# Optimization experiments

Measured on AMD Instinct MI355X. Metric: run time of the kernel, lower is better.

The kernel has to match this reference:

```python
import jax, jax.numpy as jnp
import numpy as np

B, L, DIM = 2, 2048, 768
NH, HD = 12, 64  # num_heads, head_dim; NH*HD == dim_attn == 768


def setup_inputs() -> dict:
    key = jax.random.key(0)
    ks = jax.random.split(key, 7)
    x = jax.random.normal(ks[0], (B, L, DIM), dtype=jnp.float32)
    pos_bias = jax.random.normal(ks[1], (1, NH, L, L), dtype=jnp.float32)
    Wq = jax.random.normal(ks[2], (DIM, DIM), dtype=jnp.float32) * 0.02
    Wk = jax.random.normal(ks[3], (DIM, DIM), dtype=jnp.float32) * 0.02
    Wv = jax.random.normal(ks[4], (DIM, DIM), dtype=jnp.float32) * 0.02
    Wo = jax.random.normal(ks[5], (DIM, DIM), dtype=jnp.float32) * 0.02
    mask = jax.random.randint(ks[6], (B, L), 0, 2, dtype=jnp.int32)
    return {"x": x, "pos_bias": pos_bias, "Wq": Wq, "Wk": Wk, "Wv": Wv,
            "Wo": Wo, "mask": mask}


def reference(x, pos_bias, Wq, Wk, Wv, Wo, mask):
    b, l, _ = x.shape
    # q/k/v projections (torch Linear: x @ W.T), split into heads
    q = (x @ Wq.T).reshape(b, l, NH, HD)
    k = (x @ Wk.T).reshape(b, l, NH, HD)
    v = (x @ Wv.T).reshape(b, l, NH, HD)
    # additive bias [B, H, Lq, Lk]: pos_bias broadcast + key mask -> -inf
    neg_inf = jnp.finfo(x.dtype).min
    attn_bias = jnp.broadcast_to(pos_bias, (b, NH, l, l))
    attn_bias = jnp.where(mask[:, None, None, :] == 0, neg_inf, attn_bias)
    # T5-style attention: NO 1/sqrt(d) scaling
    scores = jnp.einsum('binc,bjnc->bnij', q, k) + attn_bias
    attn = jax.nn.softmax(scores.astype(jnp.float32), axis=-1).astype(x.dtype)
    out = jnp.einsum('bnij,bjnc->binc', attn, v).reshape(b, l, NH * HD)
    return out @ Wo.T
```

## Files before the change

### kernel.cpp

```cpp
#include <hip/hip_runtime.h>
#include <math.h>

#define Bq 2
#define Lq 2048
#define DIMq 768
#define NHq 12
#define HDq 64

typedef __attribute__((ext_vector_type(8))) short short8;
typedef __attribute__((ext_vector_type(4))) short short4v;
typedef __attribute__((ext_vector_type(4))) float float4v;

static __device__ __forceinline__ short f2bf(float f) {
    union { float f; unsigned u; } v; v.f = f;
    unsigned r = (v.u + 0x7FFF + ((v.u >> 16) & 1)) >> 16;
    return (short)r;
}

__global__ __launch_bounds__(256)
void to_bf16(const float* __restrict__ x,  const float* __restrict__ wq,
             const float* __restrict__ wk, const float* __restrict__ wv,
             const float* __restrict__ wo,
             short* __restrict__ xb, short* __restrict__ wqb,
             short* __restrict__ wkb, short* __restrict__ wvb,
             short* __restrict__ wob)
{
    int blk = blockIdx.x;
    const float* s; short* d; int off;
    if      (blk <  768) { s = x;  d = xb;  off = blk * 1024; }
    else if (blk <  912) { s = wq; d = wqb; off = (blk -  768) * 1024; }
    else if (blk < 1056) { s = wk; d = wkb; off = (blk -  912) * 1024; }
    else if (blk < 1200) { s = wv; d = wvb; off = (blk - 1056) * 1024; }
    else                 { s = wo; d = wob; off = (blk - 1200) * 1024; }
    const float4* s4 = (const float4*)s;
    short4v* d4 = (short4v*)d;
#pragma unroll
    for (int i = 0; i < 4; ++i) {
        int idx = off + threadIdx.x + i * 256;
        float4 v = s4[idx];
        short4v o;
        o[0] = f2bf(v.x); o[1] = f2bf(v.y); o[2] = f2bf(v.z); o[3] = f2bf(v.w);
        d4[idx] = o;
    }
}

__global__ __launch_bounds__(256, 2)
void gemm_bf16(const short* __restrict__ A,
               const short* __restrict__ W0, const short* __restrict__ W1,
               const short* __restrict__ W2,
               short* __restrict__ D0, short* __restrict__ D1,
               short* __restrict__ D2, float* __restrict__ DF, int mode)
{
    const int z = blockIdx.z;
    const short* W = (z == 0) ? W0 : ((z == 1) ? W1 : W2);
    short* DH = (z == 0) ? D0 : ((z == 1) ? D1 : D2);

    __shared__ __align__(16) short Xs[64][72];
    __shared__ __align__(16) short Ws[64][72];

    const int tid  = threadIdx.x;
    const int wave = tid >> 6;
    const int lane = tid & 63;
    const int col  = lane & 15;
    const int quad = lane >> 4;
    const int m0 = blockIdx.y * 64, n0 = blockIdx.x * 64;

    float4v acc[4];
#pragma unroll
    for (int nt = 0; nt < 4; ++nt) acc[nt] = (float4v){0.f, 0.f, 0.f, 0.f};

    for (int k0 = 0; k0 < DIMq; k0 += 64) {
        __syncthreads();
#pragma unroll
        for (int i = 0; i < 2; ++i) {
            int idx = tid + i * 256;
            int mm = idx >> 3, ch = idx & 7;
            *(short8*)&Xs[mm][ch * 8] =
                *(const short8*)&A[(size_t)(m0 + mm) * DIMq + k0 + ch * 8];
            *(short8*)&Ws[mm][ch * 8] =
                *(const short8*)&W[(size_t)(n0 + mm) * DIMq + k0 + ch * 8];
        }
        __syncthreads();
#pragma unroll
        for (int kk = 0; kk < 2; ++kk) {
            short8 a = *(const short8*)&Xs[wave * 16 + col][kk * 32 + quad * 8];
#pragma unroll
            for (int nt = 0; nt < 4; ++nt) {
                short8 bfr = *(const short8*)&Ws[nt * 16 + col][kk * 32 + quad * 8];
                acc[nt] = __builtin_amdgcn_mfma_f32_16x16x32_bf16(a, bfr, acc[nt], 0, 0, 0);
            }
        }
    }

#pragma unroll
    for (int reg = 0; reg < 4; ++reg) {
        int m = m0 + wave * 16 + quad * 4 + reg;
#pragma unroll
        for (int nt = 0; nt < 4; ++nt) {
            int n = n0 + 16 * nt + col;
            if (mode == 1) {
                int b = m >> 11, l = m & 2047, h = n >> 6, c = n & 63;
                DH[(((size_t)(b * NHq + h)) * Lq + l) * HDq + c] = f2bf(acc[nt][reg]);
            } else {
                DF[(size_t)m * DIMq + n] = acc[nt][reg];
            }
        }
    }
}

__global__ __launch_bounds__(256, 2)
void attn_fwd_mfma(const short* __restrict__ Qh, const short* __restrict__ Kh,
                   const short* __restrict__ Vh, const float* __restrict__ pos_bias,
                   const int* __restrict__ mask, short* __restrict__ AO)
{
    const int qt = blockIdx.x;
    const int h  = blockIdx.y;
    const int b  = blockIdx.z;
    const short* Q = Qh + ((size_t)(b * NHq + h)) * Lq * HDq;
    const short* K = Kh + ((size_t)(b * NHq + h)) * Lq * HDq;
    const short* V = Vh + ((size_t)(b * NHq + h)) * Lq * HDq;
    const int* mk = mask + (size_t)b * Lq;

    __shared__ __align__(16) short Ks[64][72];
    __shared__ __align__(16) short Vt[64][72];
    __shared__ __align__(16) short Ps[64][72];

    const int tid  = threadIdx.x;
    const int wave = tid >> 6;
    const int lane = tid & 63;
    const int col  = lane & 15;
    const int quad = lane >> 4;

    short8 qa[2];
    {
        const short* qrow = Q + (size_t)(qt * 64 + wave * 16 + col) * HDq;
        qa[0] = *(const short8*)&qrow[quad * 8];
        qa[1] = *(const short8*)&qrow[32 + quad * 8];
    }

    const float* brow = pos_bias + (size_t)h * Lq * Lq
                      + (size_t)(qt * 64 + wave * 16 + quad * 4) * Lq + col;

    float bcur[4][4], bnxt[4][4];
    auto prefetch = [&](int kt, float (&bb)[4][4]) {
#pragma unroll
        for (int nt = 0; nt < 4; ++nt) {
            int mval = mk[kt * 64 + col + 16 * nt];
            float fm = (mval == 0) ? -1e30f : 0.0f;
#pragma unroll
            for (int reg = 0; reg < 4; ++reg)
                bb[nt][reg] = brow[(size_t)reg * Lq + kt * 64 + 16 * nt] + fm;
        }
    };
    prefetch(0, bcur);

    float4v Oacc[4];
    float m_run[4], l_run[4];
#pragma unroll
    for (int nt = 0; nt < 4; ++nt) Oacc[nt] = (float4v){0.f, 0.f, 0.f, 0.f};
#pragma unroll
    for (int r = 0; r < 4; ++r) { m_run[r] = -1e30f; l_run[r] = 0.f; }

    for (int kt = 0; kt < Lq / 64; ++kt) {
        __syncthreads();
        const short* Kt = K + (size_t)kt * 64 * HDq;
        const short* Vg = V + (size_t)kt * 64 * HDq;
#pragma unroll
        for (int i = 0; i < 2; ++i) {
            int idx = tid + i * 256;
            int key = idx >> 3, ch = idx & 7;
            *(short8*)&Ks[key][ch * 8] = *(const short8*)&Kt[key * HDq + ch * 8];
        }
        {
            int key = tid & 63, hg = tid >> 6;
#pragma unroll
            for (int i = 0; i < 2; ++i) {
                int c = hg + i * 4;
                short8 vv = *(const short8*)&Vg[key * HDq + c * 8];
#pragma unroll
                for (int j = 0; j < 8; ++j)
                    Vt[c * 8 + j][key] = vv[j];
            }
        }
        if (kt + 1 < Lq / 64) prefetch(kt + 1, bnxt);
        __syncthreads();

        float4v S[4];
#pragma unroll
        for (int nt = 0; nt < 4; ++nt) S[nt] = (float4v){0.f, 0.f, 0.f, 0.f};
#pragma unroll
        for (int kk = 0; kk < 2; ++kk) {
#pragma unroll
            for (int nt = 0; nt < 4; ++nt) {
                short8 bfr = *(const short8*)&Ks[nt * 16 + col][kk * 32 + quad * 8];
                S[nt] = __builtin_amdgcn_mfma_f32_16x16x32_bf16(qa[kk], bfr, S[nt], 0, 0, 0);
            }
        }

        float sc[4][4];
#pragma unroll
        for (int nt = 0; nt < 4; ++nt)
#pragma unroll
            for (int reg = 0; reg < 4; ++reg)
                sc[nt][reg] = S[nt][reg] + bcur[nt][reg];
        float tm[4];
#pragma unroll
        for (int reg = 0; reg < 4; ++reg) {
            tm[reg] = fmaxf(fmaxf(sc[0][reg], sc[1][reg]),
                            fmaxf(sc[2][reg], sc[3][reg]));
#pragma unroll
            for (int off = 1; off < 16; off <<= 1)
                tm[reg] = fmaxf(tm[reg], __shfl_xor(tm[reg], off, 64));
        }
        float alpha[4], ps[4];
#pragma unroll
        for (int reg = 0; reg < 4; ++reg) {
            float mn = fmaxf(m_run[reg], tm[reg]);
            alpha[reg] = __expf(m_run[reg] - mn);
            m_run[reg] = mn;
            ps[reg] = 0.f;
        }
#pragma unroll
        for (int nt = 0; nt < 4; ++nt)
#pragma unroll
            for (int reg = 0; reg < 4; ++reg) {
                float p = __expf(sc[nt][reg] - m_run[reg]);
                sc[nt][reg] = p;
                ps[reg] += p;
            }
#pragma unroll
        for (int reg = 0; reg < 4; ++reg) {
#pragma unroll
            for (int off = 1; off < 16; off <<= 1)
                ps[reg] += __shfl_xor(ps[reg], off, 64);
            l_run[reg] = l_run[reg] * alpha[reg] + ps[reg];
        }
#pragma unroll
        for (int nt = 0; nt < 4; ++nt)
#pragma unroll
            for (int reg = 0; reg < 4; ++reg)
                Ps[wave * 16 + quad * 4 + reg][col + 16 * nt] = f2bf(sc[nt][reg]);
#pragma unroll
        for (int nt = 0; nt < 4; ++nt)
#pragma unroll
            for (int reg = 0; reg < 4; ++reg)
                Oacc[nt][reg] *= alpha[reg];
        __syncthreads();

#pragma unroll
        for (int kk = 0; kk < 2; ++kk) {
            short8 pa = *(const short8*)&Ps[wave * 16 + col][kk * 32 + quad * 8];
#pragma unroll
            for (int nt = 0; nt < 4; ++nt) {
                short8 vb = *(const short8*)&Vt[nt * 16 + col][kk * 32 + quad * 8];
                Oacc[nt] = __builtin_amdgcn_mfma_f32_16x16x32_bf16(pa, vb, Oacc[nt], 0, 0, 0);
            }
        }
#pragma unroll
        for (int nt = 0; nt < 4; ++nt)
#pragma unroll
            for (int reg = 0; reg < 4; ++reg)
                bcur[nt][reg] = bnxt[nt][reg];
    }

    short* aorow = AO + ((size_t)b * Lq + qt * 64 + wave * 16 + quad * 4) * DIMq
                 + h * HDq + col;
#pragma unroll
    for (int reg = 0; reg < 4; ++reg) {
        float inv = 1.0f / l_run[reg];
#pragma unroll
        for (int nt = 0; nt < 4; ++nt)
            aorow[(size_t)reg * DIMq + 16 * nt] = f2bf(Oacc[nt][reg] * inv);
    }
}

extern "C" void kernel_launch(void* const* d_in, const int* in_sizes, int n_in,
                              void* d_out, int out_size, void* d_ws, size_t ws_size,
                              hipStream_t stream) {
    const float* x        = (const float*)d_in[0];
    const float* pos_bias = (const float*)d_in[1];
    const float* Wq       = (const float*)d_in[2];
    const float* Wk       = (const float*)d_in[3];
    const float* Wv       = (const float*)d_in[4];
    const float* Wo       = (const float*)d_in[5];
    const int*   mask     = (const int*)d_in[6];
    float* out = (float*)d_out;

    const size_t nX = (size_t)Bq * Lq * DIMq;
    const size_t nW = (size_t)DIMq * DIMq;
    short* xb  = (short*)d_ws;
    short* wqb = xb  + nX;
    short* wkb = wqb + nW;
    short* wvb = wkb + nW;
    short* wob = wvb + nW;
    short* Qh  = wob + nW;
    short* Kh  = Qh  + nX;
    short* Vh  = Kh  + nX;
    short* AOb = Vh  + nX;

    dim3 blk(256);
    hipLaunchKernelGGL(to_bf16, dim3(1344), blk, 0, stream,
                       x, Wq, Wk, Wv, Wo, xb, wqb, wkb, wvb, wob);

    hipLaunchKernelGGL(gemm_bf16, dim3(DIMq / 64, (Bq * Lq) / 64, 3), blk, 0, stream,
                       xb, wqb, wkb, wvb, Qh, Kh, Vh, (float*)nullptr, 1);

    hipLaunchKernelGGL(attn_fwd_mfma, dim3(Lq / 64, NHq, Bq), blk, 0, stream,
                       Qh, Kh, Vh, pos_bias, mask, AOb);

    hipLaunchKernelGGL(gemm_bf16, dim3(DIMq / 64, (Bq * Lq) / 64, 1), blk, 0, stream,
                       AOb, wob, wob, wob, (short*)nullptr, (short*)nullptr,
                       (short*)nullptr, out, 0);
}
```

Baseline: 429.1 us.

## Use 128x128 GEMM tiles with direct global-to-LDS loads and double-buffer attention K/V

The GEMM moves from 64x64 to 128x128 output tiles, with each wave computing a 64x64 sub-tile, and fills LDS with global_load_lds instead of staging through registers. The aim is more operand reuse per MFMA and fewer load instructions. The attention kernel double-buffers K and V in LDS, loading the next tile into registers while the current tile is computed and writing it to LDS after the PV MFMAs, which cuts one barrier per iteration. In exchange the GEMM uses more registers, and with unpadded LDS rows its fragment reads may hit bank conflicts. The GEMM grid also shrinks, so fewer blocks are in flight.

```diff
diff --git a/kernel.cpp b/kernel.cpp
--- a/kernel.cpp
+++ b/kernel.cpp
@@ -11,10 +11,17 @@
 typedef __attribute__((ext_vector_type(4))) short short4v;
 typedef __attribute__((ext_vector_type(4))) float float4v;
 
+typedef __attribute__((address_space(3))) unsigned int as3_u32;
+typedef __attribute__((address_space(1))) unsigned int as1_u32;
+
 static __device__ __forceinline__ short f2bf(float f) {
     union { float f; unsigned u; } v; v.f = f;
     unsigned r = (v.u + 0x7FFF + ((v.u >> 16) & 1)) >> 16;
     return (short)r;
+}
+
+static __device__ __forceinline__ void gld_lds16(const short* g, short* l) {
+    __builtin_amdgcn_global_load_lds((const as1_u32*)g, (as3_u32*)l, 16, 0, 0);
 }
 
 __global__ __launch_bounds__(256)
@@ -55,54 +62,67 @@
     const short* W = (z == 0) ? W0 : ((z == 1) ? W1 : W2);
     short* DH = (z == 0) ? D0 : ((z == 1) ? D1 : D2);
 
-    __shared__ __align__(16) short Xs[64][72];
-    __shared__ __align__(16) short Ws[64][72];
+    __shared__ __align__(16) short As[128][64];
+    __shared__ __align__(16) short Ws[128][64];
 
     const int tid  = threadIdx.x;
     const int wave = tid >> 6;
     const int lane = tid & 63;
     const int col  = lane & 15;
     const int quad = lane >> 4;
-    const int m0 = blockIdx.y * 64, n0 = blockIdx.x * 64;
-
-    float4v acc[4];
-#pragma unroll
-    for (int nt = 0; nt < 4; ++nt) acc[nt] = (float4v){0.f, 0.f, 0.f, 0.f};
+    const int wr = wave >> 1, wc = wave & 1;
+    const int m0 = blockIdx.y * 128, n0 = blockIdx.x * 128;
+
+    float4v acc[4][4];
+#pragma unroll
+    for (int mt = 0; mt < 4; ++mt)
+#pragma unroll
+        for (int nt = 0; nt < 4; ++nt) acc[mt][nt] = (float4v){0.f, 0.f, 0.f, 0.f};
+
+    const short* Ab = A + (size_t)m0 * DIMq;
+    const short* Wb = W + (size_t)n0 * DIMq;
 
     for (int k0 = 0; k0 < DIMq; k0 += 64) {
         __syncthreads();
 #pragma unroll
-        for (int i = 0; i < 2; ++i) {
-            int idx = tid + i * 256;
-            int mm = idx >> 3, ch = idx & 7;
-            *(short8*)&Xs[mm][ch * 8] =
-                *(const short8*)&A[(size_t)(m0 + mm) * DIMq + k0 + ch * 8];
-            *(short8*)&Ws[mm][ch * 8] =
-                *(const short8*)&W[(size_t)(n0 + mm) * DIMq + k0 + ch * 8];
+        for (int i = 0; i < 4; ++i) {
+            int g = i * 256 + tid;
+            int row = g >> 3, ch = g & 7;
+            gld_lds16(Ab + (size_t)row * DIMq + k0 + ch * 8, (short*)As + g * 8);
+            gld_lds16(Wb + (size_t)row * DIMq + k0 + ch * 8, (short*)Ws + g * 8);
         }
         __syncthreads();
 #pragma unroll
         for (int kk = 0; kk < 2; ++kk) {
-            short8 a = *(const short8*)&Xs[wave * 16 + col][kk * 32 + quad * 8];
-#pragma unroll
-            for (int nt = 0; nt < 4; ++nt) {
-                short8 bfr = *(const short8*)&Ws[nt * 16 + col][kk * 32 + quad * 8];
-                acc[nt] = __builtin_amdgcn_mfma_f32_16x16x32_bf16(a, bfr, acc[nt], 0, 0, 0);
-            }
-        }
-    }
-
+            short8 a[4], bfr[4];
+#pragma unroll
+            for (int mt = 0; mt < 4; ++mt)
+                a[mt] = *(const short8*)&As[wr * 64 + mt * 16 + col][kk * 32 + quad * 8];
+#pragma unroll
+            for (int nt = 0; nt < 4; ++nt)
+                bfr[nt] = *(const short8*)&Ws[wc * 64 + nt * 16 + col][kk * 32 + quad * 8];
+#pragma unroll
+            for (int mt = 0; mt < 4; ++mt)
+#pragma unroll
+                for (int nt = 0; nt < 4; ++nt)
+                    acc[mt][nt] = __builtin_amdgcn_mfma_f32_16x16x32_bf16(
+                        a[mt], bfr[nt], acc[mt][nt], 0, 0, 0);
+        }
+    }
+
+#pragma unroll
+    for (int mt = 0; mt < 4; ++mt)
 #pragma unroll
     for (int reg = 0; reg < 4; ++reg) {
-        int m = m0 + wave * 16 + quad * 4 + reg;
+        int m = m0 + wr * 64 + mt * 16 + quad * 4 + reg;
 #pragma unroll
         for (int nt = 0; nt < 4; ++nt) {
-            int n = n0 + 16 * nt + col;
+            int n = n0 + wc * 64 + nt * 16 + col;
             if (mode == 1) {
                 int b = m >> 11, l = m & 2047, h = n >> 6, c = n & 63;
-                DH[(((size_t)(b * NHq + h)) * Lq + l) * HDq + c] = f2bf(acc[nt][reg]);
+                DH[(((size_t)(b * NHq + h)) * Lq + l) * HDq + c] = f2bf(acc[mt][nt][reg]);
             } else {
-                DF[(size_t)m * DIMq + n] = acc[nt][reg];
+                DF[(size_t)m * DIMq + n] = acc[mt][nt][reg];
             }
         }
     }
@@ -121,8 +141,8 @@
     const short* V = Vh + ((size_t)(b * NHq + h)) * Lq * HDq;
     const int* mk = mask + (size_t)b * Lq;
 
-    __shared__ __align__(16) short Ks[64][72];
-    __shared__ __align__(16) short Vt[64][72];
+    __shared__ __align__(16) short Ks[2][64][72];
+    __shared__ __align__(16) short Vt[2][64][72];
     __shared__ __align__(16) short Ps[64][72];
 
     const int tid  = threadIdx.x;
@@ -152,7 +172,38 @@
                 bb[nt][reg] = brow[(size_t)reg * Lq + kt * 64 + 16 * nt] + fm;
         }
     };
-    prefetch(0, bcur);
+
+    short8 kreg[2], vreg[2];
+    auto loadKV = [&](int kt) {
+        const short* Kt = K + (size_t)kt * 64 * HDq;
+        const short* Vg = V + (size_t)kt * 64 * HDq;
+#pragma unroll
+        for (int i = 0; i < 2; ++i) {
+            int idx = tid + i * 256;
+            kreg[i] = *(const short8*)&Kt[(idx >> 3) * HDq + (idx & 7) * 8];
+        }
+        int key = tid & 63, hg = tid >> 6;
+#pragma unroll
+        for (int i = 0; i < 2; ++i) {
+            int c = hg + i * 4;
+            vreg[i] = *(const short8*)&Vg[key * HDq + c * 8];
+        }
+    };
+    auto writeKV = [&](int buf) {
+#pragma unroll
+        for (int i = 0; i < 2; ++i) {
+            int idx = tid + i * 256;
+            *(short8*)&Ks[buf][idx >> 3][(idx & 7) * 8] = kreg[i];
+        }
+        int key = tid & 63, hg = tid >> 6;
+#pragma unroll
+        for (int i = 0; i < 2; ++i) {
+            int c = hg + i * 4;
+#pragma unroll
+            for (int j = 0; j < 8; ++j)
+                Vt[buf][c * 8 + j][key] = vreg[i][j];
+        }
+    };
 
     float4v Oacc[4];
     float m_run[4], l_run[4];
@@ -161,29 +212,18 @@
 #pragma unroll
     for (int r = 0; r < 4; ++r) { m_run[r] = -1e30f; l_run[r] = 0.f; }
 
+    loadKV(0);
+    writeKV(0);
+    prefetch(0, bcur);
+    __syncthreads();
+
+    int cur = 0;
     for (int kt = 0; kt < Lq / 64; ++kt) {
-        __syncthreads();
-        const short* Kt = K + (size_t)kt * 64 * HDq;
-        const short* Vg = V + (size_t)kt * 64 * HDq;
-#pragma unroll
-        for (int i = 0; i < 2; ++i) {
-            int idx = tid + i * 256;
-            int key = idx >> 3, ch = idx & 7;
-            *(short8*)&Ks[key][ch * 8] = *(const short8*)&Kt[key * HDq + ch * 8];
-        }
-        {
-            int key = tid & 63, hg = tid >> 6;
-#pragma unroll
-            for (int i = 0; i < 2; ++i) {
-                int c = hg + i * 4;
-                short8 vv = *(const short8*)&Vg[key * HDq + c * 8];
-#pragma unroll
-                for (int j = 0; j < 8; ++j)
-                    Vt[c * 8 + j][key] = vv[j];
-            }
-        }
-        if (kt + 1 < Lq / 64) prefetch(kt + 1, bnxt);
-        __syncthreads();
+        const bool more = (kt + 1 < Lq / 64);
+        if (more) {
+            loadKV(kt + 1);
+            prefetch(kt + 1, bnxt);
+        }
 
         float4v S[4];
 #pragma unroll
@@ -192,7 +232,7 @@
         for (int kk = 0; kk < 2; ++kk) {
 #pragma unroll
             for (int nt = 0; nt < 4; ++nt) {
-                short8 bfr = *(const short8*)&Ks[nt * 16 + col][kk * 32 + quad * 8];
+                short8 bfr = *(const short8*)&Ks[cur][nt * 16 + col][kk * 32 + quad * 8];
                 S[nt] = __builtin_amdgcn_mfma_f32_16x16x32_bf16(qa[kk], bfr, S[nt], 0, 0, 0);
             }
         }
@@ -252,10 +292,14 @@
             short8 pa = *(const short8*)&Ps[wave * 16 + col][kk * 32 + quad * 8];
 #pragma unroll
             for (int nt = 0; nt < 4; ++nt) {
-                short8 vb = *(const short8*)&Vt[nt * 16 + col][kk * 32 + quad * 8];
+                short8 vb = *(const short8*)&Vt[cur][nt * 16 + col][kk * 32 + quad * 8];
                 Oacc[nt] = __builtin_amdgcn_mfma_f32_16x16x32_bf16(pa, vb, Oacc[nt], 0, 0, 0);
             }
         }
+        if (more) writeKV(cur ^ 1);
+        __syncthreads();
+        cur ^= 1;
+
 #pragma unroll
         for (int nt = 0; nt < 4; ++nt)
 #pragma unroll
@@ -302,13 +346,13 @@
     hipLaunchKernelGGL(to_bf16, dim3(1344), blk, 0, stream,
                        x, Wq, Wk, Wv, Wo, xb, wqb, wkb, wvb, wob);
 
-    hipLaunchKernelGGL(gemm_bf16, dim3(DIMq / 64, (Bq * Lq) / 64, 3), blk, 0, stream,
+    hipLaunchKernelGGL(gemm_bf16, dim3(DIMq / 128, (Bq * Lq) / 128, 3), blk, 0, stream,
                        xb, wqb, wkb, wvb, Qh, Kh, Vh, (float*)nullptr, 1);
 
     hipLaunchKernelGGL(attn_fwd_mfma, dim3(Lq / 64, NHq, Bq), blk, 0, stream,
                        Qh, Kh, Vh, pos_bias, mask, AOb);
 
-    hipLaunchKernelGGL(gemm_bf16, dim3(DIMq / 64, (Bq * Lq) / 64, 1), blk, 0, stream,
+    hipLaunchKernelGGL(gemm_bf16, dim3(DIMq / 128, (Bq * Lq) / 128, 1), blk, 0, stream,
                        AOb, wob, wob, wob, (short*)nullptr, (short*)nullptr,
                        (short*)nullptr, out, 0);
 }
```

Measured after the change: 400.4 us. 6.7% less time.
